# Optimization experiments

Hardware: AMD Instinct MI355X
Metric: run time of the kernel (lower is better)

Reference implementation:

```python
import jax, jax.numpy as jnp
import numpy as np

WINDOW = 7
TOKEN_SELF_ATTN_VALUE = -5e4  # from lucidrains local-attention
LN_EPS = 1e-5


def _layer_norm(x, g, b):
    mu = jnp.mean(x, axis=-1, keepdims=True)
    var = jnp.mean(jnp.square(x - mu), axis=-1, keepdims=True)
    return (x - mu) * jax.lax.rsqrt(var + LN_EPS) * g + b


def _local_attention(q, k, v, window):
    # q,k,v: (b, n, d); shared_qk=True, causal=True, look_backward=1, look_forward=0
    b, n, d = q.shape
    nw = n // window
    scale = d ** -0.5
    # shared_qk: l2-normalize keys (torch F.normalize eps=1e-12)
    k = k / jnp.maximum(jnp.linalg.norm(k, axis=-1, keepdims=True), 1e-12)
    bq = q.reshape(b, nw, window, d) * scale
    bk = k.reshape(b, nw, window, d)
    bv = v.reshape(b, nw, window, d)
    # look_around: previous window + current window -> (b, nw, 2w, d)
    prev_k = jnp.pad(bk, ((0, 0), (1, 0), (0, 0), (0, 0)))[:, :nw]
    prev_v = jnp.pad(bv, ((0, 0), (1, 0), (0, 0), (0, 0)))[:, :nw]
    bk2 = jnp.concatenate([prev_k, bk], axis=2)
    bv2 = jnp.concatenate([prev_v, bv], axis=2)
    # absolute positions; padded positions marked -1
    t = jnp.arange(n).reshape(nw, window)             # (nw, w)
    prev_t = jnp.pad(t, ((1, 0), (0, 0)), constant_values=-1)[:nw]
    tk = jnp.concatenate([prev_t, t], axis=1)          # (nw, 2w)
    sim = jnp.einsum('bnie,bnje->bnij', bq, bk2)       # (b, nw, w, 2w)
    self_mask = t[:, :, None] == tk[:, None, :]
    sim = jnp.where(self_mask, TOKEN_SELF_ATTN_VALUE, sim)
    invalid = (t[:, :, None] < tk[:, None, :]) | (tk[:, None, :] == -1)
    sim = jnp.where(invalid, -jnp.finfo(sim.dtype).max, sim)
    attn = jax.nn.softmax(sim, axis=-1)
    out = jnp.einsum('bnij,bnjd->bnid', attn, bv2)
    return out.reshape(b, n, d)


def setup_inputs() -> dict:
    key = jax.random.key(0)
    ks = jax.random.split(key, 10)
    B, H, W, C = 8, 112, 112, 256
    s = 1.0 / np.sqrt(C)
    return {
        'x': jax.random.normal(ks[0], (B, H, W, C), dtype=jnp.float32),
        'ln_g': jnp.ones((C,), jnp.float32),
        'ln_b': jnp.zeros((C,), jnp.float32),
        'wq_w': jax.random.uniform(ks[1], (C, C), jnp.float32, -s, s),
        'wq_b': jax.random.uniform(ks[2], (C,), jnp.float32, -s, s),
        'wk_w': jax.random.uniform(ks[3], (C, C), jnp.float32, -s, s),
        'wk_b': jax.random.uniform(ks[4], (C,), jnp.float32, -s, s),
        'wv_w': jax.random.uniform(ks[5], (C, C), jnp.float32, -s, s),
        'wv_b': jax.random.uniform(ks[6], (C,), jnp.float32, -s, s),
        'mlp_w': jax.random.uniform(ks[7], (C, C), jnp.float32, -s, s),
        'mlp_b': jax.random.uniform(ks[8], (C,), jnp.float32, -s, s),
    }


def reference(x, ln_g, ln_b, wq_w, wq_b, wk_w, wk_b, wv_w, wv_b, mlp_w, mlp_b):
    B, H, W, C = x.shape
    shift = WINDOW // 2  # int(7/2) = 3
    xs = jnp.roll(x, (shift, shift), axis=(1, 2))
    xs = _layer_norm(xs, ln_g, ln_b)
    flat = xs.reshape(B, H * W, C)
    q = flat @ wq_w.T + wq_b
    k = flat @ wk_w.T + wk_b
    v = flat @ wv_w.T + wv_b
    attn_out = _local_attention(q, k, v, WINDOW).reshape(B, H, W, C)
    x_unshifted = jnp.roll(attn_out, (-shift, -shift), axis=(1, 2))
    residual = x_unshifted + x
    xn = _layer_norm(residual, ln_g, ln_b)  # same LN params (module reused)
    flat2 = xn.reshape(B, H * W, C)
    mlp = jax.nn.gelu(flat2 @ mlp_w.T + mlp_b, approximate=False).reshape(B, H, W, C)
    return mlp + residual
```

## Files before the change

### kernel.cpp

```cpp
#include <hip/hip_runtime.h>

#define NTOK 100352
#define NPB  12544
#define CH   256

typedef unsigned short u16;
typedef float f32x4 __attribute__((ext_vector_type(4)));
typedef short bfrag __attribute__((ext_vector_type(8)));

static __device__ __forceinline__ u16 f2bf(float f) {
    union { float f; unsigned u; } v; v.f = f;
    unsigned r = v.u + 0x7FFFu + ((v.u >> 16) & 1u);
    return (u16)(r >> 16);
}
static __device__ __forceinline__ float bf2f(u16 h) {
    union { unsigned u; float f; } v; v.u = ((unsigned)h) << 16;
    return v.f;
}
static __device__ __forceinline__ unsigned pk2(float a, float b) {
    return (unsigned)f2bf(a) | ((unsigned)f2bf(b) << 16);
}
static __device__ __forceinline__ void gl16(const u16* g, u16* l) {
    __builtin_amdgcn_global_load_lds(
        (const __attribute__((address_space(1))) void*)g,
        (__attribute__((address_space(3))) void*)l, 16, 0, 0);
}

__global__ __launch_bounds__(256)
void swa_prep(const float* __restrict__ wq, const float* __restrict__ wk,
              const float* __restrict__ wv, const float* __restrict__ wm,
              u16* __restrict__ wcat, u16* __restrict__ wmb)
{
    int i0 = blockIdx.x * 256 + threadIdx.x;
    int stride = gridDim.x * 256;
    for (int i = i0; i < 768 * 256; i += stride) {
        int r = i >> 8, c = i & 255;
        float v;
        if (r < 256)      v = wq[r * 256 + c] * 0.0625f;
        else if (r < 512) v = wk[(r - 256) * 256 + c];
        else              v = wv[(r - 512) * 256 + c];
        wcat[i] = f2bf(v);
    }
    for (int i = i0; i < 256 * 256; i += stride) wmb[i] = f2bf(wm[i]);
}

__global__ __launch_bounds__(256)
void swa_ln(const float* __restrict__ x,
            const float* __restrict__ ln_g, const float* __restrict__ ln_b,
            u16* __restrict__ xn)
{
    const int lane = threadIdx.x & 63;
    const int wid  = threadIdx.x >> 6;
    f32x4 lg = *reinterpret_cast<const f32x4*>(ln_g + lane * 4);
    f32x4 lb = *reinterpret_cast<const f32x4*>(ln_b + lane * 4);

    const int wtok0 = (blockIdx.x * 4 + wid) * 16;
    for (int i = 0; i < 16; ++i) {
        int tok = wtok0 + i;
        int b_  = tok / NPB;
        int rem = tok - b_ * NPB;
        int h = rem / 112, w = rem - h * 112;
        int h0 = h - 3 + ((h < 3) ? 112 : 0);
        int w0 = w - 3 + ((w < 3) ? 112 : 0);
        f32x4 v = *reinterpret_cast<const f32x4*>(x + (size_t)(b_ * NPB + h0 * 112 + w0) * CH + lane * 4);
        float s  = v[0] + v[1] + v[2] + v[3];
        float sq = v[0]*v[0] + v[1]*v[1] + v[2]*v[2] + v[3]*v[3];
        #pragma unroll
        for (int m = 1; m < 64; m <<= 1) { s += __shfl_xor(s, m); sq += __shfl_xor(sq, m); }
        float mu  = s * (1.0f / 256.0f);
        float var = sq * (1.0f / 256.0f) - mu * mu;
        float inv = 1.0f / sqrtf(var + 1e-5f);
        uint2 p;
        p.x = pk2((v[0] - mu) * inv * lg[0] + lb[0], (v[1] - mu) * inv * lg[1] + lb[1]);
        p.y = pk2((v[2] - mu) * inv * lg[2] + lb[2], (v[3] - mu) * inv * lg[3] + lb[3]);
        *reinterpret_cast<uint2*>(xn + (size_t)tok * CH + lane * 4) = p;
    }
}

__global__ __launch_bounds__(512)
void swa_kv(const u16* __restrict__ xn, const u16* __restrict__ wcat,
            const float* __restrict__ bk, const float* __restrict__ bv,
            u16* __restrict__ kbuf, u16* __restrict__ vbuf)
{
    __shared__ u16 wt[128 * 256];

    const int tid  = threadIdx.x;
    const int lane = tid & 63;
    const int wid  = tid >> 6;
    const int r16  = lane & 15, g4 = lane >> 4;
    const int swz   = (blockIdx.x & 7) * 196 + (blockIdx.x >> 3);
    const int type  = swz / 392;
    const int strip = swz % 392;
    const int sec   = 1 + (type >> 1);
    const int half  = type & 1;
    const int tok0w = strip * 256 + wid * 32;
    const int wrow0 = sec * 256 + half * 128;

    #pragma unroll
    for (int rr2 = 0; rr2 < 8; ++rr2) {
        int o   = (tid + rr2 * 512) * 16;
        int row = o >> 9;
        int cp  = (o >> 4) & 31;
        int c   = (cp & 24) | ((cp & 7) ^ (row & 7));
        gl16(wcat + (size_t)(wrow0 + row) * CH + c * 8, wt + o / 2);
    }

    bfrag bx[2][8];
    #pragma unroll
    for (int fj = 0; fj < 2; ++fj) {
        const u16* xp = xn + (size_t)(tok0w + fj * 16 + r16) * CH + g4 * 8;
        #pragma unroll
        for (int kb = 0; kb < 8; ++kb)
            bx[fj][kb] = *reinterpret_cast<const bfrag*>(xp + kb * 32);
    }

    u16*         outp = (sec == 1) ? kbuf : vbuf;
    const float* bsp  = (sec == 1) ? bk : bv;

    __syncthreads();

    #pragma unroll
    for (int p = 0; p < 4; ++p) {
        f32x4 acc[2][2];
        #pragma unroll
        for (int ct = 0; ct < 2; ++ct) { acc[ct][0] = (f32x4)0.f; acc[ct][1] = (f32x4)0.f; }
        #pragma unroll
        for (int kk = 0; kk < 8; ++kk) {
            bfrag af[2];
            #pragma unroll
            for (int ct = 0; ct < 2; ++ct) {
                int row = p * 32 + ct * 16 + r16;
                int cc  = kk * 4 + g4;
                int cp  = (cc & 24) | ((cc & 7) ^ (row & 7));
                af[ct]  = *reinterpret_cast<const bfrag*>((const char*)wt + row * 512 + cp * 16);
            }
            #pragma unroll
            for (int ct = 0; ct < 2; ++ct) {
                acc[ct][0] = __builtin_amdgcn_mfma_f32_16x16x32_bf16(af[ct], bx[0][kk], acc[ct][0], 0, 0, 0);
                acc[ct][1] = __builtin_amdgcn_mfma_f32_16x16x32_bf16(af[ct], bx[1][kk], acc[ct][1], 0, 0, 0);
            }
        }
        #pragma unroll
        for (int ct = 0; ct < 2; ++ct) {
            int ch = half * 128 + p * 32 + ct * 16 + g4 * 4;
            f32x4 bb = *reinterpret_cast<const f32x4*>(bsp + ch);
            #pragma unroll
            for (int fj = 0; fj < 2; ++fj) {
                int tok = tok0w + fj * 16 + r16;
                uint2 pkk;
                pkk.x = pk2(acc[ct][fj][0] + bb[0], acc[ct][fj][1] + bb[1]);
                pkk.y = pk2(acc[ct][fj][2] + bb[2], acc[ct][fj][3] + bb[3]);
                *reinterpret_cast<uint2*>(outp + (size_t)tok * CH + ch) = pkk;
            }
        }
    }
}

__global__ __launch_bounds__(512)
void swa_q(u16* xnq, const u16* __restrict__ wcat, const float* __restrict__ bq)
{
    __shared__ u16 wt[256 * 256];

    const int tid  = threadIdx.x;
    const int lane = tid & 63;
    const int wid  = tid >> 6;
    const int r16  = lane & 15, g4 = lane >> 4;
    const int strip = (blockIdx.x & 7) * 49 + (blockIdx.x >> 3);
    const int tok0w = strip * 256 + wid * 32;

    #pragma unroll
    for (int rr2 = 0; rr2 < 16; ++rr2) {
        int o   = (tid + rr2 * 512) * 16;
        int row = o >> 9;
        int cp  = (o >> 4) & 31;
        int c   = (cp & 24) | ((cp & 7) ^ (row & 7));
        gl16(wcat + (size_t)row * CH + c * 8, wt + o / 2);
    }

    bfrag bx[2][8];
    #pragma unroll
    for (int fj = 0; fj < 2; ++fj) {
        const u16* xp = xnq + (size_t)(tok0w + fj * 16 + r16) * CH + g4 * 8;
        #pragma unroll
        for (int kb = 0; kb < 8; ++kb)
            bx[fj][kb] = *reinterpret_cast<const bfrag*>(xp + kb * 32);
    }

    __syncthreads();

    #pragma unroll
    for (int p = 0; p < 8; ++p) {
        f32x4 acc[2][2];
        #pragma unroll
        for (int ct = 0; ct < 2; ++ct) { acc[ct][0] = (f32x4)0.f; acc[ct][1] = (f32x4)0.f; }
        #pragma unroll
        for (int kk = 0; kk < 8; ++kk) {
            bfrag af[2];
            #pragma unroll
            for (int ct = 0; ct < 2; ++ct) {
                int row = p * 32 + ct * 16 + r16;
                int cc  = kk * 4 + g4;
                int cp  = (cc & 24) | ((cc & 7) ^ (row & 7));
                af[ct]  = *reinterpret_cast<const bfrag*>((const char*)wt + row * 512 + cp * 16);
            }
            #pragma unroll
            for (int ct = 0; ct < 2; ++ct) {
                acc[ct][0] = __builtin_amdgcn_mfma_f32_16x16x32_bf16(af[ct], bx[0][kk], acc[ct][0], 0, 0, 0);
                acc[ct][1] = __builtin_amdgcn_mfma_f32_16x16x32_bf16(af[ct], bx[1][kk], acc[ct][1], 0, 0, 0);
            }
        }
        #pragma unroll
        for (int ct = 0; ct < 2; ++ct) {
            int ch = p * 32 + ct * 16 + g4 * 4;
            f32x4 bb = *reinterpret_cast<const f32x4*>(bq + ch);
            #pragma unroll
            for (int fj = 0; fj < 2; ++fj) {
                int tok = tok0w + fj * 16 + r16;
                uint2 pkk;
                pkk.x = pk2(acc[ct][fj][0] + bb[0] * 0.0625f, acc[ct][fj][1] + bb[1] * 0.0625f);
                pkk.y = pk2(acc[ct][fj][2] + bb[2] * 0.0625f, acc[ct][fj][3] + bb[3] * 0.0625f);
                *reinterpret_cast<uint2*>(xnq + (size_t)tok * CH + ch) = pkk;
            }
        }
    }
}

__global__ __launch_bounds__(256)
void swa_attn(const u16* qbuf, const u16* kbuf, const u16* vbuf, u16* obuf)
{
    __shared__ float plds[4][16][17];
    const int tid  = threadIdx.x;
    const int lane = tid & 63;
    const int wid  = tid >> 6;
    const int win  = blockIdx.x * 4 + wid;
    const int iw   = win % 1792;
    const int base = win * 7;
    const int r16  = lane & 15;
    const int g4   = lane >> 4;

    int qrow = base + r16; if (qrow > NTOK - 1) qrow = NTOK - 1;
    int krow = base - 7 + r16; if (krow < 0) krow = 0;
    const u16* qp = qbuf + (size_t)qrow * CH + g4 * 8;
    const u16* kp = kbuf + (size_t)krow * CH + g4 * 8;

    bfrag kf[8];
    #pragma unroll
    for (int kk = 0; kk < 8; ++kk) kf[kk] = *reinterpret_cast<const bfrag*>(kp + kk * 32);
    float sq = 0.f;
    #pragma unroll
    for (int kk = 0; kk < 8; ++kk)
        #pragma unroll
        for (int e = 0; e < 8; ++e) { float kv = bf2f((u16)kf[kk][e]); sq += kv * kv; }
    sq += __shfl_xor(sq, 16); sq += __shfl_xor(sq, 32);
    float invk = 1.0f / fmaxf(sqrtf(sq), 1e-12f);

    f32x4 s4 = {0.f, 0.f, 0.f, 0.f};
    #pragma unroll
    for (int kk = 0; kk < 8; ++kk) {
        bfrag a = *reinterpret_cast<const bfrag*>(qp + kk * 32);
        s4 = __builtin_amdgcn_mfma_f32_16x16x32_bf16(a, kf[kk], s4, 0, 0, 0);
    }

    const int  j     = r16;
    const bool first = (iw == 0);
    #pragma unroll
    for (int rr = 0; rr < 4; ++rr) {
        int i = g4 * 4 + rr;
        float s = s4[rr] * invk;
        if (j == i + 7) s = -5.0e4f;
        if (j > i + 7 || j >= 14 || (first && j < 7)) s = -3.0e38f;
        s4[rr] = s;
    }
    f32x4 mx = s4;
    #pragma unroll
    for (int off = 8; off; off >>= 1) {
        #pragma unroll
        for (int rr = 0; rr < 4; ++rr) mx[rr] = fmaxf(mx[rr], __shfl_xor(mx[rr], off));
    }
    f32x4 p;
    #pragma unroll
    for (int rr = 0; rr < 4; ++rr) p[rr] = __expf(s4[rr] - mx[rr]);
    f32x4 sm = p;
    #pragma unroll
    for (int off = 8; off; off >>= 1) {
        #pragma unroll
        for (int rr = 0; rr < 4; ++rr) sm[rr] += __shfl_xor(sm[rr], off);
    }
    #pragma unroll
    for (int rr = 0; rr < 4; ++rr) plds[wid][g4 * 4 + rr][j] = p[rr] / sm[rr];
    __syncthreads();

    f32x4 zero4 = {0.f, 0.f, 0.f, 0.f};
    f32x4 oa[7];
    #pragma unroll
    for (int i = 0; i < 7; ++i) oa[i] = zero4;
    for (int jj = 0; jj < 14; ++jj) {
        int vrow = base - 7 + jj;
        if (vrow < 0) vrow = 0;
        ushort4 vr = *reinterpret_cast<const ushort4*>(vbuf + (size_t)vrow * CH + lane * 4);
        f32x4 vvv; vvv[0] = bf2f(vr.x); vvv[1] = bf2f(vr.y); vvv[2] = bf2f(vr.z); vvv[3] = bf2f(vr.w);
        #pragma unroll
        for (int i = 0; i < 7; ++i) {
            float pp = plds[wid][i][jj];
            oa[i][0] += pp * vvv[0]; oa[i][1] += pp * vvv[1];
            oa[i][2] += pp * vvv[2]; oa[i][3] += pp * vvv[3];
        }
    }
    #pragma unroll
    for (int i = 0; i < 7; ++i) {
        ushort4 o; o.x = f2bf(oa[i][0]); o.y = f2bf(oa[i][1]); o.z = f2bf(oa[i][2]); o.w = f2bf(oa[i][3]);
        *reinterpret_cast<ushort4*>(obuf + (size_t)(base + i) * CH + lane * 4) = o;
    }
}

__global__ __launch_bounds__(256)
void swa_mlp4(const float* __restrict__ x, const u16* __restrict__ abuf,
              const float* __restrict__ ln_g, const float* __restrict__ ln_b,
              const u16* __restrict__ wmb, const float* __restrict__ mbias,
              float* __restrict__ out)
{
    __shared__ u16   xs[32][264];
    __shared__ float rsd[32][260];
    __shared__ float bias[256];
    const int tid  = threadIdx.x;
    const int lane = tid & 63;
    const int wid  = tid >> 6;
    const int tok0 = blockIdx.x * 32;
    const int r16  = lane & 15;
    const int g4   = lane >> 4;

    if (tid < 256) bias[tid] = mbias[tid];
    f32x4 lg = *reinterpret_cast<const f32x4*>(ln_g + lane * 4);
    f32x4 lb = *reinterpret_cast<const f32x4*>(ln_b + lane * 4);

    for (int it = 0; it < 8; ++it) {
        int tt  = wid * 8 + it;
        int tok = tok0 + tt;
        int b_  = tok / NPB, rem = tok - b_ * NPB;
        int h = rem / 112, w = rem - h * 112;
        int hs = h + 3;  if (hs >= 112) hs -= 112;
        int ws_ = w + 3; if (ws_ >= 112) ws_ -= 112;
        const u16* arow = abuf + (size_t)(b_ * NPB + hs * 112 + ws_) * CH;
        ushort4 av = *reinterpret_cast<const ushort4*>(arow + lane * 4);
        f32x4 xv = *reinterpret_cast<const f32x4*>(x + (size_t)tok * CH + lane * 4);
        f32x4 rv;
        rv[0] = xv[0] + bf2f(av.x); rv[1] = xv[1] + bf2f(av.y);
        rv[2] = xv[2] + bf2f(av.z); rv[3] = xv[3] + bf2f(av.w);
        *reinterpret_cast<f32x4*>(&rsd[tt][lane * 4]) = rv;
        float s  = rv[0] + rv[1] + rv[2] + rv[3];
        float sq = rv[0]*rv[0] + rv[1]*rv[1] + rv[2]*rv[2] + rv[3]*rv[3];
        #pragma unroll
        for (int m = 32; m; m >>= 1) { s += __shfl_xor(s, m); sq += __shfl_xor(sq, m); }
        float mu  = s * (1.0f / 256.0f);
        float var = sq * (1.0f / 256.0f) - mu * mu;
        float inv = 1.0f / sqrtf(var + 1e-5f);
        ushort4 o;
        o.x = f2bf((rv[0] - mu) * inv * lg[0] + lb[0]);
        o.y = f2bf((rv[1] - mu) * inv * lg[1] + lb[1]);
        o.z = f2bf((rv[2] - mu) * inv * lg[2] + lb[2]);
        o.w = f2bf((rv[3] - mu) * inv * lg[3] + lb[3]);
        *reinterpret_cast<ushort4*>(&xs[tt][lane * 4]) = o;
    }
    __syncthreads();

    f32x4 acc[4][2];
    #pragma unroll
    for (int i = 0; i < 4; ++i) { acc[i][0] = (f32x4)0.f; acc[i][1] = (f32x4)0.f; }

    #pragma unroll
    for (int kk = 0; kk < 8; ++kk) {
        bfrag b0 = *reinterpret_cast<const bfrag*>(&xs[r16][kk * 32 + g4 * 8]);
        bfrag b1 = *reinterpret_cast<const bfrag*>(&xs[16 + r16][kk * 32 + g4 * 8]);
        #pragma unroll
        for (int ct = 0; ct < 4; ++ct) {
            bfrag wf = *reinterpret_cast<const bfrag*>(wmb + (size_t)(wid * 64 + ct * 16 + r16) * CH + kk * 32 + g4 * 8);
            acc[ct][0] = __builtin_amdgcn_mfma_f32_16x16x32_bf16(wf, b0, acc[ct][0], 0, 0, 0);
            acc[ct][1] = __builtin_amdgcn_mfma_f32_16x16x32_bf16(wf, b1, acc[ct][1], 0, 0, 0);
        }
    }

    #pragma unroll
    for (int ct = 0; ct < 4; ++ct) {
        int ch = wid * 64 + ct * 16 + g4 * 4;
        f32x4 bb = *reinterpret_cast<const f32x4*>(&bias[ch]);
        #pragma unroll
        for (int rt = 0; rt < 2; ++rt) {
            int tokL = rt * 16 + r16;
            f32x4 rb = *reinterpret_cast<const f32x4*>(&rsd[tokL][ch]);
            f32x4 vv;
            #pragma unroll
            for (int rr = 0; rr < 4; ++rr) {
                float val = acc[ct][rt][rr] + bb[rr];
                vv[rr] = 0.5f * val * (1.0f + erff(val * 0.70710678118654752f)) + rb[rr];
            }
            *reinterpret_cast<f32x4*>(out + (size_t)(tok0 + tokL) * CH + ch) = vv;
        }
    }
}

extern "C" void kernel_launch(void* const* d_in, const int* in_sizes, int n_in,
                              void* d_out, int out_size, void* d_ws, size_t ws_size,
                              hipStream_t stream)
{
    const float* x     = (const float*)d_in[0];
    const float* ln_g  = (const float*)d_in[1];
    const float* ln_b  = (const float*)d_in[2];
    const float* wq_w  = (const float*)d_in[3];
    const float* wq_b  = (const float*)d_in[4];
    const float* wk_w  = (const float*)d_in[5];
    const float* wk_b  = (const float*)d_in[6];
    const float* wv_w  = (const float*)d_in[7];
    const float* wv_b  = (const float*)d_in[8];
    const float* mlp_w = (const float*)d_in[9];
    const float* mlp_b = (const float*)d_in[10];

    char* ws = (char*)d_ws;
    u16* wcat = (u16*)ws;
    u16* wmb  = (u16*)(ws + 393216);
    u16* xnq  = (u16*)(ws + 524288);
    u16* kbuf = (u16*)d_out;
    u16* vbuf = (u16*)d_out + (size_t)NTOK * CH;

    swa_prep <<<256,  256, 0, stream>>>(wq_w, wk_w, wv_w, mlp_w, wcat, wmb);
    swa_ln   <<<1568, 256, 0, stream>>>(x, ln_g, ln_b, xnq);
    swa_kv   <<<1568, 512, 0, stream>>>(xnq, wcat, wk_b, wv_b, kbuf, vbuf);
    swa_q    <<<392,  512, 0, stream>>>(xnq, wcat, wq_b);
    swa_attn <<<3584, 256, 0, stream>>>(xnq, kbuf, vbuf, xnq);
    swa_mlp4 <<<3136, 256, 0, stream>>>(x, xnq, ln_g, ln_b, wmb, mlp_b, (float*)d_out);
}
```

Baseline: 269.6 us.

## Restructure MLP kernel to stage weight halves in LDS with register-held LN activations

Result: slower. 290.8 us (+7.9%).

```diff
diff --git a/kernel.cpp b/kernel.cpp
--- a/kernel.cpp
+++ b/kernel.cpp
@@ -24,6 +24,17 @@
     __builtin_amdgcn_global_load_lds(
         (const __attribute__((address_space(1))) void*)g,
         (__attribute__((address_space(3))) void*)l, 16, 0, 0);
+}
+static __device__ __forceinline__ float gelu_fast(float v) {
+    float z = v * 0.70710678118654752f;
+    float a = fabsf(z);
+    float t = 1.0f / fmaf(0.3275911f, a, 1.0f);
+    float p = t * fmaf(t, fmaf(t, fmaf(t, fmaf(t, 1.061405429f, -1.453152027f),
+                                        1.421413741f), -0.284496736f), 0.254829592f);
+    float e = __expf(-a * a);
+    float erfa = fmaf(-p, e, 1.0f);
+    float erfz = (z < 0.f) ? -erfa : erfa;
+    return 0.5f * v * (1.0f + erfz);
 }
 
 __global__ __launch_bounds__(256)
@@ -313,87 +324,112 @@
     }
 }
 
-__global__ __launch_bounds__(256)
-void swa_mlp4(const float* __restrict__ x, const u16* __restrict__ abuf,
+__global__ __launch_bounds__(512)
+void swa_mlp5(const float* __restrict__ x, const u16* __restrict__ att,
+              const u16* __restrict__ wmb, const float* __restrict__ mbias,
               const float* __restrict__ ln_g, const float* __restrict__ ln_b,
-              const u16* __restrict__ wmb, const float* __restrict__ mbias,
               float* __restrict__ out)
 {
-    __shared__ u16   xs[32][264];
-    __shared__ float rsd[32][260];
-    __shared__ float bias[256];
+    __shared__ u16 wt[128 * 256];
+
     const int tid  = threadIdx.x;
     const int lane = tid & 63;
     const int wid  = tid >> 6;
-    const int tok0 = blockIdx.x * 32;
-    const int r16  = lane & 15;
-    const int g4   = lane >> 4;
-
-    if (tid < 256) bias[tid] = mbias[tid];
-    f32x4 lg = *reinterpret_cast<const f32x4*>(ln_g + lane * 4);
-    f32x4 lb = *reinterpret_cast<const f32x4*>(ln_b + lane * 4);
-
-    for (int it = 0; it < 8; ++it) {
-        int tt  = wid * 8 + it;
-        int tok = tok0 + tt;
-        int b_  = tok / NPB, rem = tok - b_ * NPB;
-        int h = rem / 112, w = rem - h * 112;
-        int hs = h + 3;  if (hs >= 112) hs -= 112;
-        int ws_ = w + 3; if (ws_ >= 112) ws_ -= 112;
-        const u16* arow = abuf + (size_t)(b_ * NPB + hs * 112 + ws_) * CH;
-        ushort4 av = *reinterpret_cast<const ushort4*>(arow + lane * 4);
-        f32x4 xv = *reinterpret_cast<const f32x4*>(x + (size_t)tok * CH + lane * 4);
-        f32x4 rv;
-        rv[0] = xv[0] + bf2f(av.x); rv[1] = xv[1] + bf2f(av.y);
-        rv[2] = xv[2] + bf2f(av.z); rv[3] = xv[3] + bf2f(av.w);
-        *reinterpret_cast<f32x4*>(&rsd[tt][lane * 4]) = rv;
-        float s  = rv[0] + rv[1] + rv[2] + rv[3];
-        float sq = rv[0]*rv[0] + rv[1]*rv[1] + rv[2]*rv[2] + rv[3]*rv[3];
-        #pragma unroll
-        for (int m = 32; m; m >>= 1) { s += __shfl_xor(s, m); sq += __shfl_xor(sq, m); }
-        float mu  = s * (1.0f / 256.0f);
-        float var = sq * (1.0f / 256.0f) - mu * mu;
-        float inv = 1.0f / sqrtf(var + 1e-5f);
-        ushort4 o;
-        o.x = f2bf((rv[0] - mu) * inv * lg[0] + lb[0]);
-        o.y = f2bf((rv[1] - mu) * inv * lg[1] + lb[1]);
-        o.z = f2bf((rv[2] - mu) * inv * lg[2] + lb[2]);
-        o.w = f2bf((rv[3] - mu) * inv * lg[3] + lb[3]);
-        *reinterpret_cast<ushort4*>(&xs[tt][lane * 4]) = o;
-    }
+    const int r16  = lane & 15, g4 = lane >> 4;
+    const int swz   = (blockIdx.x & 7) * 196 + (blockIdx.x >> 3);
+    const int half  = swz / 784;
+    const int strip = swz % 784;
+    const int tok   = strip * 128 + wid * 16 + r16;
+
+    #pragma unroll
+    for (int rr2 = 0; rr2 < 8; ++rr2) {
+        int o   = (tid + rr2 * 512) * 16;
+        int row = o >> 9;
+        int cp  = (o >> 4) & 31;
+        int c   = (cp & 24) | ((cp & 7) ^ (row & 7));
+        gl16(wmb + (size_t)(half * 128 + row) * CH + c * 8, wt + o / 2);
+    }
+
+    int b_  = tok / NPB, rem = tok - b_ * NPB;
+    int h = rem / 112, w = rem - h * 112;
+    int hs = h + 3;  if (hs >= 112) hs -= 112;
+    int ws_ = w + 3; if (ws_ >= 112) ws_ -= 112;
+    const float* xrow = x + (size_t)tok * CH;
+    const u16*   arow = att + (size_t)(b_ * NPB + hs * 112 + ws_) * CH;
+
+    f32x4 rv[16];
+    #pragma unroll
+    for (int kb = 0; kb < 8; ++kb) {
+        int off = g4 * 8 + kb * 32;
+        f32x4 x0 = *reinterpret_cast<const f32x4*>(xrow + off);
+        f32x4 x1 = *reinterpret_cast<const f32x4*>(xrow + off + 4);
+        ushort4 a0 = *reinterpret_cast<const ushort4*>(arow + off);
+        ushort4 a1 = *reinterpret_cast<const ushort4*>(arow + off + 4);
+        rv[kb*2][0]   = x0[0] + bf2f(a0.x); rv[kb*2][1]   = x0[1] + bf2f(a0.y);
+        rv[kb*2][2]   = x0[2] + bf2f(a0.z); rv[kb*2][3]   = x0[3] + bf2f(a0.w);
+        rv[kb*2+1][0] = x1[0] + bf2f(a1.x); rv[kb*2+1][1] = x1[1] + bf2f(a1.y);
+        rv[kb*2+1][2] = x1[2] + bf2f(a1.z); rv[kb*2+1][3] = x1[3] + bf2f(a1.w);
+    }
+    float s = 0.f, sq = 0.f;
+    #pragma unroll
+    for (int q = 0; q < 16; ++q) {
+        s  += rv[q][0] + rv[q][1] + rv[q][2] + rv[q][3];
+        sq += rv[q][0]*rv[q][0] + rv[q][1]*rv[q][1] + rv[q][2]*rv[q][2] + rv[q][3]*rv[q][3];
+    }
+    s  += __shfl_xor(s, 16); sq += __shfl_xor(sq, 16);
+    s  += __shfl_xor(s, 32); sq += __shfl_xor(sq, 32);
+    float mu  = s * (1.0f / 256.0f);
+    float var = sq * (1.0f / 256.0f) - mu * mu;
+    float inv = 1.0f / sqrtf(var + 1e-5f);
+
+    bfrag bx[8];
+    #pragma unroll
+    for (int kb = 0; kb < 8; ++kb) {
+        int off = g4 * 8 + kb * 32;
+        f32x4 g0 = *reinterpret_cast<const f32x4*>(ln_g + off);
+        f32x4 g1 = *reinterpret_cast<const f32x4*>(ln_g + off + 4);
+        f32x4 b0 = *reinterpret_cast<const f32x4*>(ln_b + off);
+        f32x4 b1 = *reinterpret_cast<const f32x4*>(ln_b + off + 4);
+        f32x4 a0 = rv[kb*2], a1 = rv[kb*2+1];
+        union { unsigned u[4]; bfrag f; } cv;
+        cv.u[0] = pk2((a0[0]-mu)*inv*g0[0]+b0[0], (a0[1]-mu)*inv*g0[1]+b0[1]);
+        cv.u[1] = pk2((a0[2]-mu)*inv*g0[2]+b0[2], (a0[3]-mu)*inv*g0[3]+b0[3]);
+        cv.u[2] = pk2((a1[0]-mu)*inv*g1[0]+b1[0], (a1[1]-mu)*inv*g1[1]+b1[1]);
+        cv.u[3] = pk2((a1[2]-mu)*inv*g1[2]+b1[2], (a1[3]-mu)*inv*g1[3]+b1[3]);
+        bx[kb] = cv.f;
+    }
+
     __syncthreads();
 
-    f32x4 acc[4][2];
-    #pragma unroll
-    for (int i = 0; i < 4; ++i) { acc[i][0] = (f32x4)0.f; acc[i][1] = (f32x4)0.f; }
-
-    #pragma unroll
-    for (int kk = 0; kk < 8; ++kk) {
-        bfrag b0 = *reinterpret_cast<const bfrag*>(&xs[r16][kk * 32 + g4 * 8]);
-        bfrag b1 = *reinterpret_cast<const bfrag*>(&xs[16 + r16][kk * 32 + g4 * 8]);
-        #pragma unroll
-        for (int ct = 0; ct < 4; ++ct) {
-            bfrag wf = *reinterpret_cast<const bfrag*>(wmb + (size_t)(wid * 64 + ct * 16 + r16) * CH + kk * 32 + g4 * 8);
-            acc[ct][0] = __builtin_amdgcn_mfma_f32_16x16x32_bf16(wf, b0, acc[ct][0], 0, 0, 0);
-            acc[ct][1] = __builtin_amdgcn_mfma_f32_16x16x32_bf16(wf, b1, acc[ct][1], 0, 0, 0);
-        }
-    }
-
-    #pragma unroll
-    for (int ct = 0; ct < 4; ++ct) {
-        int ch = wid * 64 + ct * 16 + g4 * 4;
-        f32x4 bb = *reinterpret_cast<const f32x4*>(&bias[ch]);
-        #pragma unroll
-        for (int rt = 0; rt < 2; ++rt) {
-            int tokL = rt * 16 + r16;
-            f32x4 rb = *reinterpret_cast<const f32x4*>(&rsd[tokL][ch]);
-            f32x4 vv;
-            #pragma unroll
-            for (int rr = 0; rr < 4; ++rr) {
-                float val = acc[ct][rt][rr] + bb[rr];
-                vv[rr] = 0.5f * val * (1.0f + erff(val * 0.70710678118654752f)) + rb[rr];
-            }
-            *reinterpret_cast<f32x4*>(out + (size_t)(tok0 + tokL) * CH + ch) = vv;
+    #pragma unroll
+    for (int p = 0; p < 4; ++p) {
+        f32x4 acc[2];
+        acc[0] = (f32x4)0.f; acc[1] = (f32x4)0.f;
+        #pragma unroll
+        for (int kk = 0; kk < 8; ++kk) {
+            bfrag af[2];
+            #pragma unroll
+            for (int ct = 0; ct < 2; ++ct) {
+                int row = p * 32 + ct * 16 + r16;
+                int cc  = kk * 4 + g4;
+                int cp  = (cc & 24) | ((cc & 7) ^ (row & 7));
+                af[ct]  = *reinterpret_cast<const bfrag*>((const char*)wt + row * 512 + cp * 16);
+            }
+            acc[0] = __builtin_amdgcn_mfma_f32_16x16x32_bf16(af[0], bx[kk], acc[0], 0, 0, 0);
+            acc[1] = __builtin_amdgcn_mfma_f32_16x16x32_bf16(af[1], bx[kk], acc[1], 0, 0, 0);
+        }
+        #pragma unroll
+        for (int ct = 0; ct < 2; ++ct) {
+            int ch = half * 128 + p * 32 + ct * 16 + g4 * 4;
+            f32x4 bb = *reinterpret_cast<const f32x4*>(mbias + ch);
+            f32x4 xr = *reinterpret_cast<const f32x4*>(xrow + ch);
+            ushort4 ar = *reinterpret_cast<const ushort4*>(arow + ch);
+            f32x4 ov;
+            ov[0] = gelu_fast(acc[ct][0] + bb[0]) + xr[0] + bf2f(ar.x);
+            ov[1] = gelu_fast(acc[ct][1] + bb[1]) + xr[1] + bf2f(ar.y);
+            ov[2] = gelu_fast(acc[ct][2] + bb[2]) + xr[2] + bf2f(ar.z);
+            ov[3] = gelu_fast(acc[ct][3] + bb[3]) + xr[3] + bf2f(ar.w);
+            *reinterpret_cast<f32x4*>(out + (size_t)tok * CH + ch) = ov;
         }
     }
 }
@@ -426,5 +462,5 @@
     swa_kv   <<<1568, 512, 0, stream>>>(xnq, wcat, wk_b, wv_b, kbuf, vbuf);
     swa_q    <<<392,  512, 0, stream>>>(xnq, wcat, wq_b);
     swa_attn <<<3584, 256, 0, stream>>>(xnq, kbuf, vbuf, xnq);
-    swa_mlp4 <<<3136, 256, 0, stream>>>(x, xnq, ln_g, ln_b, wmb, mlp_b, (float*)d_out);
-}
+    swa_mlp5 <<<1568, 512, 0, stream>>>(x, xnq, wmb, mlp_b, ln_g, ln_b, (float*)d_out);
+}
```
